# Optimization experiments

Measured on AMD Instinct MI355X. Metric: run time of the kernel, lower is better.

The kernel has to match this reference:

```python
import jax, jax.numpy as jnp
import numpy as np

B, HEADS, SCALES, POINTS, HIDDEN = 1, 8, 4, 4, 192
HEAD_DIM = HIDDEN // HEADS
OFFSET_SCALE = 0.35
EPS = 1e-5


def conv1x1(x, W, b=None):
    # x: [B,C,D,H,W], W: [O,C]
    y = jnp.einsum('bcdhw,oc->bodhw', x, W)
    if b is not None:
        y = y + b[None, :, None, None, None]
    return y


def base_grid(D, H, W, dtype):
    z = jnp.linspace(-1.0, 1.0, D, dtype=dtype)
    y = jnp.linspace(-1.0, 1.0, H, dtype=dtype)
    x = jnp.linspace(-1.0, 1.0, W, dtype=dtype)
    zz, yy, xx = jnp.meshgrid(z, y, x, indexing='ij')
    return jnp.stack((xx, yy, zz), axis=-1)  # [D,H,W,3] (x,y,z order)


def trilinear_sample(val, grid):
    # val: [BH,C,Dv,Hv,Wv]; grid: [BH,N,3] normalized (x,y,z), align_corners=False, border padding
    BH, C, Dv, Hv, Wv = val.shape
    unnorm = lambda g, s: jnp.clip(((g + 1.0) * s - 1.0) * 0.5, 0.0, s - 1.0)
    ix = unnorm(grid[..., 0], Wv)
    iy = unnorm(grid[..., 1], Hv)
    iz = unnorm(grid[..., 2], Dv)
    x0f, y0f, z0f = jnp.floor(ix), jnp.floor(iy), jnp.floor(iz)
    wx, wy, wz = ix - x0f, iy - y0f, iz - z0f
    x0 = x0f.astype(jnp.int32); x1 = jnp.minimum(x0 + 1, Wv - 1)
    y0 = y0f.astype(jnp.int32); y1 = jnp.minimum(y0 + 1, Hv - 1)
    z0 = z0f.astype(jnp.int32); z1 = jnp.minimum(z0 + 1, Dv - 1)
    vflat = val.reshape(BH, C, Dv * Hv * Wv)
    gather = jax.vmap(lambda v, i: v[:, i])  # -> [BH,C,N]
    def corner(zi, yi, xi):
        return gather(vflat, (zi * Hv + yi) * Wv + xi)
    w = lambda a: a[:, None, :]  # broadcast weight over channel dim
    out = (corner(z0, y0, x0) * w((1 - wz) * (1 - wy) * (1 - wx))
           + corner(z0, y0, x1) * w((1 - wz) * (1 - wy) * wx)
           + corner(z0, y1, x0) * w((1 - wz) * wy * (1 - wx))
           + corner(z0, y1, x1) * w((1 - wz) * wy * wx)
           + corner(z1, y0, x0) * w(wz * (1 - wy) * (1 - wx))
           + corner(z1, y0, x1) * w(wz * (1 - wy) * wx)
           + corner(z1, y1, x0) * w(wz * wy * (1 - wx))
           + corner(z1, y1, x1) * w(wz * wy * wx))
    return out


def fsad_forward(query_feature, values, Wq, Wvs, Woff, boff, Wwt, bwt, Wout, gamma, beta):
    Bq, _, D, H, W = query_feature.shape
    N = D * H * W
    q = conv1x1(query_feature, Wq)
    off = conv1x1(q, Woff, boff).reshape(Bq, HEADS, SCALES, POINTS, 3, D, H, W)
    off = jnp.tanh(off) * OFFSET_SCALE
    aw = conv1x1(q, Wwt, bwt).reshape(Bq, HEADS, SCALES * POINTS, D, H, W)
    aw = jax.nn.softmax(aw, axis=2).reshape(Bq, HEADS, SCALES, POINTS, D, H, W)
    bg = base_grid(D, H, W, q.dtype)  # [D,H,W,3]
    acc = jnp.zeros((Bq, HEADS, HEAD_DIM, D, H, W), q.dtype)
    for s in range(SCALES):
        feat = values[s]
        val = conv1x1(feat, Wvs[s]).reshape(Bq * HEADS, HEAD_DIM, *feat.shape[2:])
        # off[:,:,s]: [B,Hh,P,3,D,H,W] -> grid [B,Hh,P,D,H,W,3]
        grid = bg[None, None, None] + jnp.moveaxis(off[:, :, s], 3, -1)
        grid = grid.reshape(Bq * HEADS, POINTS * N, 3)
        sampled = trilinear_sample(val, grid).reshape(Bq, HEADS, HEAD_DIM, POINTS, D, H, W)
        acc = acc + jnp.einsum('bhcpdyx,bhpdyx->bhcdyx', sampled, aw[:, :, s])
    out = conv1x1(acc.reshape(Bq, HIDDEN, D, H, W), Wout)
    # InstanceNorm3d(affine=True)
    mu = out.mean(axis=(2, 3, 4), keepdims=True)
    var = out.var(axis=(2, 3, 4), keepdims=True)
    out = (out - mu) * jax.lax.rsqrt(var + EPS)
    return out * gamma[None, :, None, None, None] + beta[None, :, None, None, None]


def setup_inputs() -> dict:
    key = jax.random.key(0)
    ks = jax.random.split(key, 16)
    value_channels = [32, 64, 128, 256]
    sizes = [64, 32, 16, 8]
    inp = {
        'query_feature': jax.random.normal(ks[0], (1, 128, 16, 16, 16), jnp.float32),
        'v0': jax.random.normal(ks[1], (1, 32, 64, 64, 64), jnp.float32),
        'v1': jax.random.normal(ks[2], (1, 64, 32, 32, 32), jnp.float32),
        'v2': jax.random.normal(ks[3], (1, 128, 16, 16, 16), jnp.float32),
        'v3': jax.random.normal(ks[4], (1, 256, 8, 8, 8), jnp.float32),
        'Wq': jax.random.normal(ks[5], (HIDDEN, 128), jnp.float32) * 0.05,
        'Wv0': jax.random.normal(ks[6], (HIDDEN, 32), jnp.float32) * 0.05,
        'Wv1': jax.random.normal(ks[7], (HIDDEN, 64), jnp.float32) * 0.05,
        'Wv2': jax.random.normal(ks[8], (HIDDEN, 128), jnp.float32) * 0.05,
        'Wv3': jax.random.normal(ks[9], (HIDDEN, 256), jnp.float32) * 0.05,
        'Woff': jax.random.normal(ks[10], (HEADS * SCALES * POINTS * 3, HIDDEN), jnp.float32) * 0.05,
        'boff': jnp.zeros((HEADS * SCALES * POINTS * 3,), jnp.float32),
        'Wwt': jax.random.normal(ks[11], (HEADS * SCALES * POINTS, HIDDEN), jnp.float32) * 0.05,
        'bwt': jnp.zeros((HEADS * SCALES * POINTS,), jnp.float32),
        'Wout': jax.random.normal(ks[12], (128, HIDDEN), jnp.float32) * 0.05,
        'gamma': jnp.ones((128,), jnp.float32),
        'beta': jnp.zeros((128,), jnp.float32),
    }
    return inp


def reference(query_feature, v0, v1, v2, v3, Wq, Wv0, Wv1, Wv2, Wv3, Woff, boff, Wwt, bwt, Wout, gamma, beta):
    return fsad_forward(query_feature, [v0, v1, v2, v3], Wq, [Wv0, Wv1, Wv2, Wv3], Woff, boff, Wwt, bwt, Wout, gamma, beta)
```

## Files before the change

kernel.cpp:

```cpp
#include <hip/hip_runtime.h>
#include <hip/hip_fp16.h>
#include <cmath>

#define N_Q 4096
#define HEADS 8
#define HEAD_DIM 24
#define HIDDEN 192

__device__ __forceinline__ float4 ld4(const float* p) { return *(const float4*)p; }

__device__ __forceinline__ void fma8h(float* u, float w, const __half* p) {
    uint4 raw = *(const uint4*)p;
    const __half2* h2 = reinterpret_cast<const __half2*>(&raw);
#pragma unroll
    for (int k = 0; k < 4; k++) {
        float2 f = __half22float2(h2[k]);
        u[2 * k]     = fmaf(w, f.x, u[2 * k]);
        u[2 * k + 1] = fmaf(w, f.y, u[2 * k + 1]);
    }
}

__device__ __forceinline__ void corner24(float* acc, float w, const __half* p) {
    fma8h(acc,      w, p);
    fma8h(acc + 8,  w, p + 8);
    fma8h(acc + 16, w, p + 16);
}


__device__ __forceinline__ void transpose_body(char* smem, const float* __restrict__ src,
                                               __half* __restrict__ dst, int bx, int tid)
{
    float (*lds)[33] = (float(*)[33])smem;
    const int Nv = 262144;
    int pos0 = bx * 256;
    for (int k = tid; k < 256 * 32; k += 256) {
        int c = k >> 8, p = k & 255;
        lds[p][c] = src[(size_t)c * Nv + pos0 + p];
    }
    __syncthreads();
    for (int k = tid; k < 256 * 32; k += 256) {
        int p = k >> 5, c = k & 31;
        dst[(size_t)(pos0 + p) * 32 + c] = __float2half(lds[p][c]);
    }
}

template<int C, int OG>
__device__ __forceinline__ void valconv_body(char* smem, const float* __restrict__ Wv,
                                             const float* __restrict__ v,
                                             __half* __restrict__ valT, int Nv,
                                             int bx, int by, int tid)
{
    float* Wl = (float*)smem;
    __half* outs = (__half*)(smem + OG * C * 4);
    int p0 = bx * 64;
    int og0 = by * OG;
    for (int k = tid; k < OG * C; k += 256) Wl[k] = Wv[(size_t)(og0 + k / C) * C + (k % C)];
    __syncthreads();

    int osub = tid >> 6;
    int lane = tid & 63;
    constexpr int PT = OG / 4;
    float acc[PT];
#pragma unroll
    for (int i = 0; i < PT; i++) acc[i] = 0.f;
    for (int c = 0; c < C; c++) {
        float vv = v[(size_t)c * Nv + p0 + lane];
#pragma unroll
        for (int i = 0; i < PT; i++)
            acc[i] = fmaf(Wl[(osub * PT + i) * C + c], vv, acc[i]);
    }
#pragma unroll
    for (int i = 0; i < PT; i++)
        outs[lane * OG + osub * PT + i] = __float2half(acc[i]);
    __syncthreads();

    unsigned int* dst = (unsigned int*)valT;
    const unsigned int* src = (const unsigned int*)outs;
    constexpr int UPP = OG / 2;
    for (int k = tid; k < 64 * UPP; k += 256) {
        int p = k / UPP, i = k % UPP;
        dst[(size_t)(p0 + p) * (HIDDEN / 2) + (og0 / 2) + i] = src[p * UPP + i];
    }
}

__device__ __forceinline__ void wcomb_body(int bx, int tid,
                                           const float* __restrict__ Woff,
                                           const float* __restrict__ Wwt,
                                           const float* __restrict__ Wq,
                                           const float* __restrict__ boff,
                                           const float* __restrict__ bwt,
                                           float* __restrict__ Wcomb,
                                           float* __restrict__ biasc)
{
    int o = bx * 2 + (tid >> 7);
    int c = tid & 127;
    const float* A = (o < 384) ? (Woff + (size_t)o * 192) : (Wwt + (size_t)(o - 384) * 192);
    float s = 0.f;
#pragma unroll 4
    for (int k = 0; k < 192; k++) s = fmaf(A[k], Wq[k * 128 + c], s);
    Wcomb[(size_t)o * 128 + c] = s;
    if (c == 0) biasc[o] = (o < 384) ? boff[o] : bwt[o - 384];
}

__global__ __launch_bounds__(256)
void prep_kernel(const float* __restrict__ v0, __half* __restrict__ v0T,
                 const float* __restrict__ Wv1, const float* __restrict__ v1, __half* __restrict__ val1T,
                 const float* __restrict__ Wv2, const float* __restrict__ v2, __half* __restrict__ val2T,
                 const float* __restrict__ Wv3, const float* __restrict__ v3, __half* __restrict__ val3T,
                 const float* __restrict__ Woff, const float* __restrict__ Wwt,
                 const float* __restrict__ Wq, const float* __restrict__ boff,
                 const float* __restrict__ bwt, float* __restrict__ Wcomb,
                 float* __restrict__ biasc)
{
    __shared__ __align__(16) char smem[33792];
    int id = blockIdx.x;
    int tid = threadIdx.x;
    if (id < 1024) {
        transpose_body(smem, v0, v0T, id, tid);
    } else if (id < 5120) {
        int i1 = id - 1024;
        valconv_body<64, 24>(smem, Wv1, v1, val1T, 32768, i1 & 511, i1 >> 9, tid);
    } else if (id < 6144) {
        int i2 = id - 5120;
        valconv_body<128, 12>(smem, Wv2, v2, val2T, 4096, i2 & 63, i2 >> 6, tid);
    } else if (id < 6336) {
        int i3 = id - 6144;
        valconv_body<256, 8>(smem, Wv3, v3, val3T, 512, i3 & 7, i3 >> 3, tid);
    } else {
        wcomb_body(id - 6336, tid, Woff, Wwt, Wq, boff, bwt, Wcomb, biasc);
    }
}

__global__ __launch_bounds__(256)
void offaw_kernel(const float* __restrict__ Wcomb, const float* __restrict__ biasc,
                  const float* __restrict__ qf, float* __restrict__ ob)
{
    __shared__ float xs[128 * 64];
    __shared__ float Wl[32 * 128];
    __shared__ float ls[32 * 64];
    int tid = threadIdx.x;
    int n0 = blockIdx.x * 64;
    int og0 = blockIdx.y * 32;
    for (int k = tid; k < 128 * 64; k += 256) xs[k] = qf[(size_t)(k >> 6) * N_Q + n0 + (k & 63)];
    for (int k = tid; k < 32 * 128; k += 256) Wl[k] = Wcomb[(size_t)og0 * 128 + k];
    __syncthreads();

    int wv = tid >> 6, lane = tid & 63;
    float acc[8];
#pragma unroll
    for (int i = 0; i < 8; i++) acc[i] = 0.f;
    for (int c = 0; c < 128; c++) {
        float xv = xs[c * 64 + lane];
#pragma unroll
        for (int i = 0; i < 8; i++)
            acc[i] = fmaf(Wl[(wv * 8 + i) * 128 + c], xv, acc[i]);
    }

    if (og0 < 384) {
#pragma unroll
        for (int i = 0; i < 8; i++) {
            int o = og0 + wv * 8 + i;
            ob[(size_t)o * N_Q + n0 + lane] = tanhf(acc[i] + biasc[o]) * 0.35f;
        }
    } else {
#pragma unroll
        for (int i = 0; i < 8; i++) {
            int o = og0 + wv * 8 + i;
            ls[(wv * 8 + i) * 64 + lane] = acc[i] + biasc[o];
        }
        __syncthreads();
        if (tid < 128) {
            int hl = tid >> 6;
            int n2 = tid & 63;
            float v[16];
            float m = -1e30f;
#pragma unroll
            for (int j = 0; j < 16; j++) { v[j] = ls[(hl * 16 + j) * 64 + n2]; m = fmaxf(m, v[j]); }
            float ssum = 0.f;
#pragma unroll
            for (int j = 0; j < 16; j++) { v[j] = __expf(v[j] - m); ssum += v[j]; }
            float inv = 1.0f / ssum;
            int orow = og0 + hl * 16;
#pragma unroll
            for (int j = 0; j < 16; j++)
                ob[(size_t)(orow + j) * N_Q + n0 + n2] = v[j] * inv;
        }
    }
}

__global__ __launch_bounds__(256)
void sample_kernel(const float* __restrict__ offb, const float* __restrict__ awb,
                   const __half* __restrict__ v0T, const __half* __restrict__ val1T,
                   const __half* __restrict__ val2T, const __half* __restrict__ val3T,
                   const float* __restrict__ Wv0,
                   __half* __restrict__ accb)
{
    int tid = threadIdx.x;
    int id = blockIdx.x;
    int t = id & 15;
    int h = (id >> 4) & 7;
    int sp = id >> 7;
    int n = t * 256 + tid;
    int s = sp >> 2, p = sp & 3;

    int wx = n & 15, hy = (n >> 4) & 15, dz = n >> 8;
    const float step = 2.0f / 15.0f;
    float bx = -1.f + wx * step;
    float by = -1.f + hy * step;
    float bz = -1.f + dz * step;

    float acc[HEAD_DIM];
#pragma unroll
    for (int j = 0; j < HEAD_DIM; j++) acc[j] = 0.f;

    int S = 64;
    const __half* srcT = v0T;
    if (s == 1)      { S = 32; srcT = val1T; }
    else if (s == 2) { S = 16; srcT = val2T; }
    else if (s == 3) { S = 8;  srcT = val3T; }
    float fS = (float)S;

    int orow = ((h * 4 + s) * 4 + p) * 3;
    float ox = offb[(orow + 0) * N_Q + n];
    float oy = offb[(orow + 1) * N_Q + n];
    float oz = offb[(orow + 2) * N_Q + n];
    float awv = awb[(h * 16 + s * 4 + p) * N_Q + n];

    float ix = fminf(fmaxf(((bx + ox + 1.f) * fS - 1.f) * 0.5f, 0.f), fS - 1.f);
    float iy = fminf(fmaxf(((by + oy + 1.f) * fS - 1.f) * 0.5f, 0.f), fS - 1.f);
    float iz = fminf(fmaxf(((bz + oz + 1.f) * fS - 1.f) * 0.5f, 0.f), fS - 1.f);

    float x0f = floorf(ix), y0f = floorf(iy), z0f = floorf(iz);
    float fx = ix - x0f, fy = iy - y0f, fz = iz - z0f;
    int x0 = (int)x0f, y0 = (int)y0f, z0 = (int)z0f;
    int x1 = min(x0 + 1, S - 1), y1 = min(y0 + 1, S - 1), z1 = min(z0 + 1, S - 1);

    int r000 = (z0 * S + y0) * S + x0, r001 = (z0 * S + y0) * S + x1;
    int r010 = (z0 * S + y1) * S + x0, r011 = (z0 * S + y1) * S + x1;
    int r100 = (z1 * S + y0) * S + x0, r101 = (z1 * S + y0) * S + x1;
    int r110 = (z1 * S + y1) * S + x0, r111 = (z1 * S + y1) * S + x1;

    float gx1 = fx, gx0 = 1.f - fx;
    float gy1 = fy, gy0 = 1.f - fy;
    float gz1 = fz, gz0 = 1.f - fz;
    float w000 = gz0 * gy0 * gx0 * awv, w001 = gz0 * gy0 * gx1 * awv;
    float w010 = gz0 * gy1 * gx0 * awv, w011 = gz0 * gy1 * gx1 * awv;
    float w100 = gz1 * gy0 * gx0 * awv, w101 = gz1 * gy0 * gx1 * awv;
    float w110 = gz1 * gy1 * gx0 * awv, w111 = gz1 * gy1 * gx1 * awv;

    if (s == 0) {
        const float* Wvh = Wv0 + h * HEAD_DIM * 32;
#pragma unroll
        for (int c8 = 0; c8 < 32; c8 += 8) {
            float u[8] = {0.f, 0.f, 0.f, 0.f, 0.f, 0.f, 0.f, 0.f};
            fma8h(u, w000, srcT + r000 * 32 + c8);
            fma8h(u, w001, srcT + r001 * 32 + c8);
            fma8h(u, w010, srcT + r010 * 32 + c8);
            fma8h(u, w011, srcT + r011 * 32 + c8);
            fma8h(u, w100, srcT + r100 * 32 + c8);
            fma8h(u, w101, srcT + r101 * 32 + c8);
            fma8h(u, w110, srcT + r110 * 32 + c8);
            fma8h(u, w111, srcT + r111 * 32 + c8);
#pragma unroll
            for (int j = 0; j < HEAD_DIM; j++) {
                const float* wp = Wvh + j * 32 + c8;
                float4 wa = ld4(wp), wb = ld4(wp + 4);
                acc[j] = fmaf(wa.x, u[0], fmaf(wa.y, u[1], fmaf(wa.z, u[2], fmaf(wa.w, u[3],
                         fmaf(wb.x, u[4], fmaf(wb.y, u[5], fmaf(wb.z, u[6], fmaf(wb.w, u[7], acc[j]))))))));
            }
        }
    } else {
        const __half* base = srcT + h * HEAD_DIM;
        corner24(acc, w000, base + (size_t)r000 * HIDDEN);
        corner24(acc, w001, base + (size_t)r001 * HIDDEN);
        corner24(acc, w010, base + (size_t)r010 * HIDDEN);
        corner24(acc, w011, base + (size_t)r011 * HIDDEN);
        corner24(acc, w100, base + (size_t)r100 * HIDDEN);
        corner24(acc, w101, base + (size_t)r101 * HIDDEN);
        corner24(acc, w110, base + (size_t)r110 * HIDDEN);
        corner24(acc, w111, base + (size_t)r111 * HIDDEN);
    }

    __half* ab = accb + (size_t)sp * HIDDEN * N_Q;
#pragma unroll
    for (int j = 0; j < HEAD_DIM; j++) ab[(h * HEAD_DIM + j) * N_Q + n] = __float2half(acc[j]);
}

__global__ __launch_bounds__(256)
void accsum_kernel(const __half* __restrict__ accb, float* __restrict__ accsum)
{
    int i = blockIdx.x * 256 + threadIdx.x;
    const int SB8 = HIDDEN * N_Q / 8;
    const uint4* src = (const uint4*)accb;
    float a[8] = {0.f, 0.f, 0.f, 0.f, 0.f, 0.f, 0.f, 0.f};
#pragma unroll
    for (int sp = 0; sp < 16; sp++) {
        uint4 r = src[sp * SB8 + i];
        const __half2* h2 = (const __half2*)&r;
#pragma unroll
        for (int k = 0; k < 4; k++) {
            float2 f = __half22float2(h2[k]);
            a[2 * k] += f.x; a[2 * k + 1] += f.y;
        }
    }
    float4* dst = (float4*)accsum;
    dst[i * 2]     = make_float4(a[0], a[1], a[2], a[3]);
    dst[i * 2 + 1] = make_float4(a[4], a[5], a[6], a[7]);
}

__global__ __launch_bounds__(256)
void outconv_kernel(const float* __restrict__ Wout, const float* __restrict__ accsum,
                    float* __restrict__ out)
{
    __shared__ float xs[HIDDEN * 64];
    __shared__ float Wl[32 * HIDDEN];
    int tid = threadIdx.x;
    int n0 = blockIdx.x * 64;
    int og0 = blockIdx.y * 32;
    for (int k = tid; k < HIDDEN * 64; k += 256) xs[k] = accsum[(size_t)(k >> 6) * N_Q + n0 + (k & 63)];
    for (int k = tid; k < 32 * HIDDEN; k += 256) Wl[k] = Wout[(size_t)og0 * HIDDEN + k];
    __syncthreads();

    int wv = tid >> 6, lane = tid & 63;
    float acc[8];
#pragma unroll
    for (int i = 0; i < 8; i++) acc[i] = 0.f;
    for (int c = 0; c < HIDDEN; c++) {
        float xv = xs[c * 64 + lane];
#pragma unroll
        for (int i = 0; i < 8; i++)
            acc[i] = fmaf(Wl[(wv * 8 + i) * HIDDEN + c], xv, acc[i]);
    }
#pragma unroll
    for (int i = 0; i < 8; i++)
        out[(size_t)(og0 + wv * 8 + i) * N_Q + n0 + lane] = acc[i];
}

__global__ __launch_bounds__(256)
void inorm_kernel(float* __restrict__ out, const float* __restrict__ gamma,
                  const float* __restrict__ beta)
{
    int o = blockIdx.x;
    int tid = threadIdx.x;
    float s = 0.f, s2 = 0.f;
    for (int n = tid; n < N_Q; n += 256) {
        float v = out[o * N_Q + n];
        s += v; s2 += v * v;
    }
    __shared__ float rs[256], rs2[256];
    rs[tid] = s; rs2[tid] = s2;
    __syncthreads();
    for (int k = 128; k > 0; k >>= 1) {
        if (tid < k) { rs[tid] += rs[tid + k]; rs2[tid] += rs2[tid + k]; }
        __syncthreads();
    }
    float mu = rs[0] * (1.0f / N_Q);
    float var = rs2[0] * (1.0f / N_Q) - mu * mu;
    float rstd = rsqrtf(var + 1e-5f);
    float g = gamma[o] * rstd;
    float b = beta[o] - mu * g;
    for (int n = tid; n < N_Q; n += 256) {
        out[o * N_Q + n] = fmaf(out[o * N_Q + n], g, b);
    }
}

extern "C" void kernel_launch(void* const* d_in, const int* in_sizes, int n_in,
                              void* d_out, int out_size, void* d_ws, size_t ws_size,
                              hipStream_t stream)
{
    const float* qf    = (const float*)d_in[0];
    const float* v0    = (const float*)d_in[1];
    const float* v1    = (const float*)d_in[2];
    const float* v2    = (const float*)d_in[3];
    const float* v3    = (const float*)d_in[4];
    const float* Wq    = (const float*)d_in[5];
    const float* Wv0   = (const float*)d_in[6];
    const float* Wv1   = (const float*)d_in[7];
    const float* Wv2   = (const float*)d_in[8];
    const float* Wv3   = (const float*)d_in[9];
    const float* Woff  = (const float*)d_in[10];
    const float* boff  = (const float*)d_in[11];
    const float* Wwt   = (const float*)d_in[12];
    const float* bwt   = (const float*)d_in[13];
    const float* Wout  = (const float*)d_in[14];
    const float* gamma = (const float*)d_in[15];
    const float* beta  = (const float*)d_in[16];
    float* out = (float*)d_out;

    float* ws     = (float*)d_ws;
    float*  Wcomb  = ws;
    float*  biasc  = Wcomb  + 65536;
    float*  offb   = biasc  + 512;
    float*  awb    = offb   + 384 * 4096;
    __half* v0T    = (__half*)(offb + 2097152);
    __half* val1T  = (__half*)((float*)v0T + 4194304);
    __half* val2T  = (__half*)((float*)val1T + 3145728);
    __half* val3T  = (__half*)((float*)val2T + 393216);
    __half* accb   = (__half*)((float*)val3T + 49152);
    float*  accsum = (float*)accb + 6291456;

    prep_kernel<<<6592, 256, 0, stream>>>(v0, v0T, Wv1, v1, val1T, Wv2, v2, val2T,
                                          Wv3, v3, val3T, Woff, Wwt, Wq, boff, bwt,
                                          Wcomb, biasc);
    offaw_kernel<<<dim3(64, 16), 256, 0, stream>>>(Wcomb, biasc, qf, offb);
    sample_kernel<<<2048, 256, 0, stream>>>(offb, awb, v0T, val1T, val2T, val3T, Wv0, accb);
    accsum_kernel<<<384, 256, 0, stream>>>(accb, accsum);
    outconv_kernel<<<dim3(64, 4), 256, 0, stream>>>(Wout, accsum, out);
    inorm_kernel<<<128, 256, 0, stream>>>(out, gamma, beta);
}
```

Before: 257.3 us.

## Head-major value layout, larger valconv tiles, reordered sample blocks, fp16 accsum, wider outconv

Stores projected value volumes head-major ([head][voxel][24]) so each head's trilinear corner reads come from a compact contiguous region instead of 192-wide rows. The value-projection blocks now cover more output channels each (fewer blocks, fewer repeated reads of the input volume), and the sample kernel's block-to-(scale,head,point,tile) mapping is reordered to improve cache locality. The accumulated sum is stored as fp16 to halve traffic into outconv, which now computes 64 output channels per block. Risks include more shared memory per prep block (lower occupancy), precision loss from the fp16 accsum, and strided per-head writes in valconv.

After: 279.9 us. 8.8% more time.

```diff
diff --git a/kernel.cpp b/kernel.cpp
--- a/kernel.cpp
+++ b/kernel.cpp
@@ -63,6 +63,7 @@
     float acc[PT];
 #pragma unroll
     for (int i = 0; i < PT; i++) acc[i] = 0.f;
+#pragma unroll 2
     for (int c = 0; c < C; c++) {
         float vv = v[(size_t)c * Nv + p0 + lane];
 #pragma unroll
@@ -79,7 +80,9 @@
     constexpr int UPP = OG / 2;
     for (int k = tid; k < 64 * UPP; k += 256) {
         int p = k / UPP, i = k % UPP;
-        dst[(size_t)(p0 + p) * (HIDDEN / 2) + (og0 / 2) + i] = src[p * UPP + i];
+        int hh = og0 / 24 + i / 12;
+        int ii = i % 12;
+        dst[((size_t)hh * Nv + p0 + p) * 12 + ii] = src[p * UPP + i];
     }
 }
 
@@ -112,22 +115,22 @@
                  const float* __restrict__ bwt, float* __restrict__ Wcomb,
                  float* __restrict__ biasc)
 {
-    __shared__ __align__(16) char smem[33792];
+    __shared__ __align__(16) char smem[61440];
     int id = blockIdx.x;
     int tid = threadIdx.x;
     if (id < 1024) {
         transpose_body(smem, v0, v0T, id, tid);
-    } else if (id < 5120) {
+    } else if (id < 2048) {
         int i1 = id - 1024;
-        valconv_body<64, 24>(smem, Wv1, v1, val1T, 32768, i1 & 511, i1 >> 9, tid);
-    } else if (id < 6144) {
-        int i2 = id - 5120;
-        valconv_body<128, 12>(smem, Wv2, v2, val2T, 4096, i2 & 63, i2 >> 6, tid);
-    } else if (id < 6336) {
-        int i3 = id - 6144;
-        valconv_body<256, 8>(smem, Wv3, v3, val3T, 512, i3 & 7, i3 >> 3, tid);
+        valconv_body<64, 96>(smem, Wv1, v1, val1T, 32768, i1 & 511, i1 >> 9, tid);
+    } else if (id < 2176) {
+        int i2 = id - 2048;
+        valconv_body<128, 96>(smem, Wv2, v2, val2T, 4096, i2 & 63, i2 >> 6, tid);
+    } else if (id < 2208) {
+        int i3 = id - 2176;
+        valconv_body<256, 48>(smem, Wv3, v3, val3T, 512, i3 & 7, i3 >> 3, tid);
     } else {
-        wcomb_body(id - 6336, tid, Woff, Wwt, Wq, boff, bwt, Wcomb, biasc);
+        wcomb_body(id - 2208, tid, Woff, Wwt, Wq, boff, bwt, Wcomb, biasc);
     }
 }
 
@@ -197,11 +200,20 @@
 {
     int tid = threadIdx.x;
     int id = blockIdx.x;
-    int t = id & 15;
-    int h = (id >> 4) & 7;
-    int sp = id >> 7;
+    int s, h, p, t;
+    if (id < 512) {
+        s = 0; int r = id & 7; int j = id >> 3;
+        t = r + 8 * (j >> 5);
+        int rest = j & 31; h = rest >> 2; p = rest & 3;
+    } else if (id < 1024) {
+        s = 1; int i = id - 512; h = i & 7;
+        int j = i >> 3; t = j & 15; p = j >> 4;
+    } else {
+        int i = id - 1024; s = 2 + (i >> 9);
+        int i2 = i & 511; t = i2 & 15; p = (i2 >> 4) & 3; h = i2 >> 6;
+    }
     int n = t * 256 + tid;
-    int s = sp >> 2, p = sp & 3;
+    int sp = s * 4 + p;
 
     int wx = n & 15, hy = (n >> 4) & 15, dz = n >> 8;
     const float step = 2.0f / 15.0f;
@@ -270,15 +282,16 @@
             }
         }
     } else {
-        const __half* base = srcT + h * HEAD_DIM;
-        corner24(acc, w000, base + (size_t)r000 * HIDDEN);
-        corner24(acc, w001, base + (size_t)r001 * HIDDEN);
-        corner24(acc, w010, base + (size_t)r010 * HIDDEN);
-        corner24(acc, w011, base + (size_t)r011 * HIDDEN);
-        corner24(acc, w100, base + (size_t)r100 * HIDDEN);
-        corner24(acc, w101, base + (size_t)r101 * HIDDEN);
-        corner24(acc, w110, base + (size_t)r110 * HIDDEN);
-        corner24(acc, w111, base + (size_t)r111 * HIDDEN);
+        int NvS = S * S * S;
+        const __half* base = srcT + (size_t)h * NvS * HEAD_DIM;
+        corner24(acc, w000, base + (size_t)r000 * HEAD_DIM);
+        corner24(acc, w001, base + (size_t)r001 * HEAD_DIM);
+        corner24(acc, w010, base + (size_t)r010 * HEAD_DIM);
+        corner24(acc, w011, base + (size_t)r011 * HEAD_DIM);
+        corner24(acc, w100, base + (size_t)r100 * HEAD_DIM);
+        corner24(acc, w101, base + (size_t)r101 * HEAD_DIM);
+        corner24(acc, w110, base + (size_t)r110 * HEAD_DIM);
+        corner24(acc, w111, base + (size_t)r111 * HEAD_DIM);
     }
 
     __half* ab = accb + (size_t)sp * HIDDEN * N_Q;
@@ -287,7 +300,7 @@
 }
 
 __global__ __launch_bounds__(256)
-void accsum_kernel(const __half* __restrict__ accb, float* __restrict__ accsum)
+void accsum_kernel(const __half* __restrict__ accb, __half* __restrict__ accsum)
 {
     int i = blockIdx.x * 256 + threadIdx.x;
     const int SB8 = HIDDEN * N_Q / 8;
@@ -303,37 +316,50 @@
             a[2 * k] += f.x; a[2 * k + 1] += f.y;
         }
     }
-    float4* dst = (float4*)accsum;
-    dst[i * 2]     = make_float4(a[0], a[1], a[2], a[3]);
-    dst[i * 2 + 1] = make_float4(a[4], a[5], a[6], a[7]);
-}
-
-__global__ __launch_bounds__(256)
-void outconv_kernel(const float* __restrict__ Wout, const float* __restrict__ accsum,
+    uint4 o;
+    __half2* oh = (__half2*)&o;
+#pragma unroll
+    for (int k = 0; k < 4; k++)
+        oh[k] = __float22half2_rn(make_float2(a[2 * k], a[2 * k + 1]));
+    ((uint4*)accsum)[i] = o;
+}
+
+__global__ __launch_bounds__(256)
+void outconv_kernel(const float* __restrict__ Wout, const __half* __restrict__ accsum,
                     float* __restrict__ out)
 {
     __shared__ float xs[HIDDEN * 64];
-    __shared__ float Wl[32 * HIDDEN];
+    __shared__ float Wl[64 * HIDDEN];
     int tid = threadIdx.x;
     int n0 = blockIdx.x * 64;
-    int og0 = blockIdx.y * 32;
-    for (int k = tid; k < HIDDEN * 64; k += 256) xs[k] = accsum[(size_t)(k >> 6) * N_Q + n0 + (k & 63)];
-    for (int k = tid; k < 32 * HIDDEN; k += 256) Wl[k] = Wout[(size_t)og0 * HIDDEN + k];
+    int og0 = blockIdx.y * 64;
+    for (int k = tid; k < HIDDEN * 8; k += 256) {
+        int c = k >> 3, seg = k & 7;
+        uint4 r = *(const uint4*)(accsum + (size_t)c * N_Q + n0 + seg * 8);
+        const __half2* h2 = (const __half2*)&r;
+#pragma unroll
+        for (int j = 0; j < 4; j++) {
+            float2 f = __half22float2(h2[j]);
+            xs[c * 64 + seg * 8 + 2 * j]     = f.x;
+            xs[c * 64 + seg * 8 + 2 * j + 1] = f.y;
+        }
+    }
+    for (int k = tid; k < 64 * HIDDEN; k += 256) Wl[k] = Wout[(size_t)og0 * HIDDEN + k];
     __syncthreads();
 
     int wv = tid >> 6, lane = tid & 63;
-    float acc[8];
-#pragma unroll
-    for (int i = 0; i < 8; i++) acc[i] = 0.f;
+    float acc[16];
+#pragma unroll
+    for (int i = 0; i < 16; i++) acc[i] = 0.f;
     for (int c = 0; c < HIDDEN; c++) {
         float xv = xs[c * 64 + lane];
 #pragma unroll
-        for (int i = 0; i < 8; i++)
-            acc[i] = fmaf(Wl[(wv * 8 + i) * HIDDEN + c], xv, acc[i]);
-    }
-#pragma unroll
-    for (int i = 0; i < 8; i++)
-        out[(size_t)(og0 + wv * 8 + i) * N_Q + n0 + lane] = acc[i];
+        for (int i = 0; i < 16; i++)
+            acc[i] = fmaf(Wl[(wv * 16 + i) * HIDDEN + c], xv, acc[i]);
+    }
+#pragma unroll
+    for (int i = 0; i < 16; i++)
+        out[(size_t)(og0 + wv * 16 + i) * N_Q + n0 + lane] = acc[i];
 }
 
 __global__ __launch_bounds__(256)
@@ -397,14 +423,14 @@
     __half* val2T  = (__half*)((float*)val1T + 3145728);
     __half* val3T  = (__half*)((float*)val2T + 393216);
     __half* accb   = (__half*)((float*)val3T + 49152);
-    float*  accsum = (float*)accb + 6291456;
-
-    prep_kernel<<<6592, 256, 0, stream>>>(v0, v0T, Wv1, v1, val1T, Wv2, v2, val2T,
+    __half* accsum = accb + 12582912;
+
+    prep_kernel<<<2464, 256, 0, stream>>>(v0, v0T, Wv1, v1, val1T, Wv2, v2, val2T,
                                           Wv3, v3, val3T, Woff, Wwt, Wq, boff, bwt,
                                           Wcomb, biasc);
     offaw_kernel<<<dim3(64, 16), 256, 0, stream>>>(Wcomb, biasc, qf, offb);
     sample_kernel<<<2048, 256, 0, stream>>>(offb, awb, v0T, val1T, val2T, val3T, Wv0, accb);
     accsum_kernel<<<384, 256, 0, stream>>>(accb, accsum);
-    outconv_kernel<<<dim3(64, 4), 256, 0, stream>>>(Wout, accsum, out);
+    outconv_kernel<<<dim3(64, 2), 256, 0, stream>>>(Wout, accsum, out);
     inorm_kernel<<<128, 256, 0, stream>>>(out, gamma, beta);
 }
```
